# Kernel optimization log

Measured on AMD Instinct MI355X. Metric: run time of the kernel, lower is better.

The kernel has to match this reference:

```python
import jax, jax.numpy as jnp
import numpy as np

V = 100000   # vocab_size
D = 128      # d_model
N = 262144   # number of (target, context) training pairs
K = 5        # num_negatives


def setup_inputs() -> dict:
    key = jax.random.key(0)
    k1, k2, k3, k4, k5 = jax.random.split(key, 5)
    emb = jax.random.normal(k1, (V, D), dtype=jnp.float32)      # input embedding table
    out_w = jax.random.normal(k2, (V, D), dtype=jnp.float32)    # output (Linear) weight [V, D]
    tgt_ids = jax.random.randint(k3, (N,), 0, V)
    ctx_ids = jax.random.randint(k4, (N,), 0, V)
    neg_ids = jax.random.randint(k5, (N, K), 0, V)
    return {"emb": emb, "out_w": out_w, "tgt_ids": tgt_ids,
            "ctx_ids": ctx_ids, "neg_ids": neg_ids}


def reference(emb, out_w, tgt_ids, ctx_ids, neg_ids):
    # Batched skip-gram with negative sampling (SGNS), faithful to the
    # per-pair math in _train_skipgram:
    #   input_e = embeddings(tgt); pos_e = weight.weight[ctx]
    #   neg_e   = weight.weight[neg_ids]
    #   loss    = -(logsigmoid(<input_e, pos_e>) + sum logsigmoid(-neg_e @ input_e))
    input_e = emb[tgt_ids]            # [N, D]
    pos_e = out_w[ctx_ids]            # [N, D]
    neg_e = out_w[neg_ids]            # [N, K, D]

    pos_score = jnp.sum(input_e * pos_e, axis=-1)            # [N]
    neg_score = jnp.einsum('nkd,nd->nk', neg_e, input_e)     # [N, K]

    loss = -(jax.nn.log_sigmoid(pos_score)
             + jnp.sum(jax.nn.log_sigmoid(-neg_score), axis=-1))  # [N]
    return loss
```

## Files before the change

kernel.cpp:

```cpp
#include <hip/hip_runtime.h>
#include <hip/hip_fp16.h>
#include <math.h>


#define D 128
#define K 5

typedef _Float16 h2 __attribute__((ext_vector_type(2)));

__device__ __forceinline__ void sched_fence() {
#if __has_builtin(__builtin_amdgcn_sched_barrier)
    __builtin_amdgcn_sched_barrier(0);
#else
    asm volatile("" ::: "memory");
#endif
}

__device__ __forceinline__ float log_sigmoid(float x) {
    return fminf(x, 0.0f) - __logf(1.0f + __expf(-fabsf(x)));
}

__device__ __forceinline__ float dot8_f16(uint4 a, uint4 b, float acc) {
    acc = __builtin_amdgcn_fdot2(__builtin_bit_cast(h2, a.x),
                                 __builtin_bit_cast(h2, b.x), acc, false);
    acc = __builtin_amdgcn_fdot2(__builtin_bit_cast(h2, a.y),
                                 __builtin_bit_cast(h2, b.y), acc, false);
    acc = __builtin_amdgcn_fdot2(__builtin_bit_cast(h2, a.z),
                                 __builtin_bit_cast(h2, b.z), acc, false);
    acc = __builtin_amdgcn_fdot2(__builtin_bit_cast(h2, a.w),
                                 __builtin_bit_cast(h2, b.w), acc, false);
    return acc;
}

struct H8 { __half2 a, b, c, d; };

__global__ __launch_bounds__(256) void cvt2_f16_kernel(
    const float* __restrict__ src0, const float* __restrict__ src1,
    __half* __restrict__ dst0, __half* __restrict__ dst1, int n )
{
    int i = (blockIdx.x * blockDim.x + threadIdx.x) * 8;
    const float* src = src0;
    __half* dst = dst0;
    if (i >= n) { src = src1; dst = dst1; i -= n; }
    if (i >= n) return;
    float4 x = *(const float4*)(src + i);
    float4 y = *(const float4*)(src + i + 4);
    H8 h;
    h.a = __floats2half2_rn(x.x, x.y);
    h.b = __floats2half2_rn(x.z, x.w);
    h.c = __floats2half2_rn(y.x, y.y);
    h.d = __floats2half2_rn(y.z, y.w);
    *(H8*)(dst + i) = h;
}

__global__ __launch_bounds__(256) void sgns_f16_kernel(
    const __half* __restrict__ embh,
    const __half* __restrict__ outh,
    const int* __restrict__ tgt_ids,
    const int* __restrict__ ctx_ids,
    const int* __restrict__ neg_ids,
    float* __restrict__ out,
    int N)
{
    const int lane = threadIdx.x & 63;
    const int wave = threadIdx.x >> 6;
    const int lg   = lane & 15;
    const int grp  = lane >> 4;
    const int base = (blockIdx.x * 4 + wave) * 8;
    const int n0 = base + grp;
    const int n1 = n0 + 4;
    if (n0 >= N) return;

    const int t0 = tgt_ids[n0];
    const int t1 = tgt_ids[n1];
    int rowsA[K + 1], rowsB[K + 1];
    rowsA[0] = ctx_ids[n0];
    rowsB[0] = ctx_ids[n1];
    {
        const int4 a4 = *(const int4*)(neg_ids + (size_t)n0 * K);
        rowsA[1] = a4.x; rowsA[2] = a4.y; rowsA[3] = a4.z; rowsA[4] = a4.w;
        rowsA[5] = neg_ids[(size_t)n0 * K + 4];
        const int4 b4 = *(const int4*)(neg_ids + (size_t)n1 * K);
        rowsB[1] = b4.x; rowsB[2] = b4.y; rowsB[3] = b4.z; rowsB[4] = b4.w;
        rowsB[5] = neg_ids[(size_t)n1 * K + 4];
    }

    const uint4 inA = ((const uint4*)(embh + (size_t)t0 * D))[lg];
    const uint4 inB = ((const uint4*)(embh + (size_t)t1 * D))[lg];
    uint4 wA[K + 1], wB[K + 1];
#pragma unroll
    for (int j = 0; j < K + 1; ++j)
        wA[j] = ((const uint4*)(outh + (size_t)rowsA[j] * D))[lg];
#pragma unroll
    for (int j = 0; j < K + 1; ++j)
        wB[j] = ((const uint4*)(outh + (size_t)rowsB[j] * D))[lg];
    sched_fence();

    float dotA[K + 1], dotB[K + 1];
#pragma unroll
    for (int j = 0; j < K + 1; ++j)
        dotA[j] = dot8_f16(inA, wA[j], 0.0f);
#pragma unroll
    for (int j = 0; j < K + 1; ++j)
        dotB[j] = dot8_f16(inB, wB[j], 0.0f);

#pragma unroll
    for (int j = 0; j < K + 1; ++j) {
        float v = dotA[j];
        v += __shfl_xor(v, 1);
        v += __shfl_xor(v, 2);
        v += __shfl_xor(v, 4);
        v += __shfl_xor(v, 8);
        dotA[j] = v;
        float u = dotB[j];
        u += __shfl_xor(u, 1);
        u += __shfl_xor(u, 2);
        u += __shfl_xor(u, 4);
        u += __shfl_xor(u, 8);
        dotB[j] = u;
    }

    if (lg == 0) {
        float lossA = log_sigmoid(dotA[0]);
        float lossB = log_sigmoid(dotB[0]);
#pragma unroll
        for (int j = 1; j < K + 1; ++j) {
            lossA += log_sigmoid(-dotA[j]);
            lossB += log_sigmoid(-dotB[j]);
        }
        out[n0] = -lossA;
        out[n1] = -lossB;
    }
}

__global__ __launch_bounds__(256) void sgns_f32_kernel(
    const float* __restrict__ emb,
    const float* __restrict__ out_w,
    const int* __restrict__ tgt_ids,
    const int* __restrict__ ctx_ids,
    const int* __restrict__ neg_ids,
    float* __restrict__ out,
    int N)
{
    const int lane = threadIdx.x & 63;
    const int wave = threadIdx.x >> 6;
    const int lg   = lane & 15;
    const int grp  = lane >> 4;
    const int n = (blockIdx.x * 4 + wave) * 4 + grp;
    if (n >= N) return;

    const int t = tgt_ids[n];
    int rows[K + 1];
    rows[0] = ctx_ids[n];
    const int4 n4 = *(const int4*)(neg_ids + (size_t)n * K);
    rows[1] = n4.x; rows[2] = n4.y; rows[3] = n4.z; rows[4] = n4.w;
    rows[5] = neg_ids[(size_t)n * K + 4];

    const float4* er = (const float4*)(emb + (size_t)t * D);
    const float4 in0 = er[lg];
    const float4 in1 = er[lg + 16];

    float4 w0[K + 1], w1[K + 1];
#pragma unroll
    for (int j = 0; j < K + 1; ++j) {
        const float4* wr = (const float4*)(out_w + (size_t)rows[j] * D);
        w0[j] = wr[lg];
        w1[j] = wr[lg + 16];
    }

    float dot[K + 1];
#pragma unroll
    for (int j = 0; j < K + 1; ++j) {
        dot[j] = in0.x * w0[j].x + in0.y * w0[j].y
               + in0.z * w0[j].z + in0.w * w0[j].w
               + in1.x * w1[j].x + in1.y * w1[j].y
               + in1.z * w1[j].z + in1.w * w1[j].w;
    }

#pragma unroll
    for (int j = 0; j < K + 1; ++j) {
        float v = dot[j];
        v += __shfl_xor(v, 1);
        v += __shfl_xor(v, 2);
        v += __shfl_xor(v, 4);
        v += __shfl_xor(v, 8);
        dot[j] = v;
    }

    if (lg == 0) {
        float loss = log_sigmoid(dot[0]);
#pragma unroll
        for (int j = 1; j < K + 1; ++j)
            loss += log_sigmoid(-dot[j]);
        out[n] = -loss;
    }
}

extern "C" void kernel_launch(void* const* d_in, const int* in_sizes, int n_in,
                              void* d_out, int out_size, void* d_ws, size_t ws_size,
                              hipStream_t stream) {
    const float* emb     = (const float*)d_in[0];
    const float* out_w   = (const float*)d_in[1];
    const int*   tgt_ids = (const int*)d_in[2];
    const int*   ctx_ids = (const int*)d_in[3];
    const int*   neg_ids = (const int*)d_in[4];
    float* out = (float*)d_out;

    const int N = in_sizes[2];
    const size_t vd = (size_t)in_sizes[0];
    const size_t need = 2 * vd * sizeof(__half);

    if (ws_size >= need) {
        __half* embh = (__half*)d_ws;
        __half* outh = embh + vd;
        const int cvt_threads = (int)(2 * vd / 8);
        const int cvt_blocks = (cvt_threads + 255) / 256;
        cvt2_f16_kernel<<<cvt_blocks, 256, 0, stream>>>(emb, out_w, embh, outh,
                                                        (int)vd);
        const int blocks = (N + 31) / 32;
        sgns_f16_kernel<<<blocks, 256, 0, stream>>>(embh, outh, tgt_ids,
                                                    ctx_ids, neg_ids, out, N);
    } else {
        const int blocks = (N + 15) / 16;
        sgns_f32_kernel<<<blocks, 256, 0, stream>>>(emb, out_w, tgt_ids,
                                                    ctx_ids, neg_ids, out, N);
    }
}
```

Measured before the change: 191.5 us.

## Gather embedding rows via direct global-to-LDS loads, one pair per lane group

Replaces the register-based gather of f16 embedding rows with global_load_lds builtins that copy 16-byte fragments straight into per-wave shared memory, then reads them back from LDS for the fdot2 dot products. Each 16-lane group now handles one pair instead of two, so the grid doubles and out-of-range threads are clamped instead of returning early. The aim is to cut VGPR pressure and raise the number of loads in flight. The cost is 28 KB of LDS per block, which may cap occupancy, plus an extra LDS read pass and less per-thread memory-level parallelism.

```diff
diff --git a/kernel.cpp b/kernel.cpp
--- a/kernel.cpp
+++ b/kernel.cpp
@@ -7,14 +7,6 @@
 #define K 5
 
 typedef _Float16 h2 __attribute__((ext_vector_type(2)));
-
-__device__ __forceinline__ void sched_fence() {
-#if __has_builtin(__builtin_amdgcn_sched_barrier)
-    __builtin_amdgcn_sched_barrier(0);
-#else
-    asm volatile("" ::: "memory");
-#endif
-}
 
 __device__ __forceinline__ float log_sigmoid(float x) {
     return fminf(x, 0.0f) - __logf(1.0f + __expf(-fabsf(x)));
@@ -30,6 +22,13 @@
     acc = __builtin_amdgcn_fdot2(__builtin_bit_cast(h2, a.w),
                                  __builtin_bit_cast(h2, b.w), acc, false);
     return acc;
+}
+
+__device__ __forceinline__ void gload16(const void* gptr, void* lptr) {
+    __builtin_amdgcn_global_load_lds(
+        (const __attribute__((address_space(1))) void*)gptr,
+        (__attribute__((address_space(3))) void*)lptr,
+        16, 0, 0);
 }
 
 struct H8 { __half2 a, b, c, d; };
@@ -53,7 +52,7 @@
     *(H8*)(dst + i) = h;
 }
 
-__global__ __launch_bounds__(256) void sgns_f16_kernel(
+__global__ __launch_bounds__(256) void sgns_f16_lds_kernel(
     const __half* __restrict__ embh,
     const __half* __restrict__ outh,
     const int* __restrict__ tgt_ids,
@@ -62,74 +61,63 @@
     float* __restrict__ out,
     int N)
 {
+    __shared__ alignas(16) char smem[4 * 7 * 1024];
+
     const int lane = threadIdx.x & 63;
     const int wave = threadIdx.x >> 6;
     const int lg   = lane & 15;
     const int grp  = lane >> 4;
-    const int base = (blockIdx.x * 4 + wave) * 8;
-    const int n0 = base + grp;
-    const int n1 = n0 + 4;
-    if (n0 >= N) return;
-
-    const int t0 = tgt_ids[n0];
-    const int t1 = tgt_ids[n1];
-    int rowsA[K + 1], rowsB[K + 1];
-    rowsA[0] = ctx_ids[n0];
-    rowsB[0] = ctx_ids[n1];
+    const int n_raw = (blockIdx.x * 4 + wave) * 4 + grp;
+    const bool valid = n_raw < N;
+    const int n = valid ? n_raw : N - 1;
+
+    const int t = tgt_ids[n];
+    int rows[K + 1];
+    rows[0] = ctx_ids[n];
     {
-        const int4 a4 = *(const int4*)(neg_ids + (size_t)n0 * K);
-        rowsA[1] = a4.x; rowsA[2] = a4.y; rowsA[3] = a4.z; rowsA[4] = a4.w;
-        rowsA[5] = neg_ids[(size_t)n0 * K + 4];
-        const int4 b4 = *(const int4*)(neg_ids + (size_t)n1 * K);
-        rowsB[1] = b4.x; rowsB[2] = b4.y; rowsB[3] = b4.z; rowsB[4] = b4.w;
-        rowsB[5] = neg_ids[(size_t)n1 * K + 4];
-    }
-
-    const uint4 inA = ((const uint4*)(embh + (size_t)t0 * D))[lg];
-    const uint4 inB = ((const uint4*)(embh + (size_t)t1 * D))[lg];
-    uint4 wA[K + 1], wB[K + 1];
+        const int4 n4 = *(const int4*)(neg_ids + (size_t)n * K);
+        rows[1] = n4.x; rows[2] = n4.y; rows[3] = n4.z; rows[4] = n4.w;
+        rows[5] = neg_ids[(size_t)n * K + 4];
+    }
+
+    char* wbase = smem + wave * (7 * 1024);
+
+    gload16(embh + (size_t)t * D + lg * 8, wbase);
 #pragma unroll
     for (int j = 0; j < K + 1; ++j)
-        wA[j] = ((const uint4*)(outh + (size_t)rowsA[j] * D))[lg];
-#pragma unroll
-    for (int j = 0; j < K + 1; ++j)
-        wB[j] = ((const uint4*)(outh + (size_t)rowsB[j] * D))[lg];
-    sched_fence();
-
-    float dotA[K + 1], dotB[K + 1];
-#pragma unroll
-    for (int j = 0; j < K + 1; ++j)
-        dotA[j] = dot8_f16(inA, wA[j], 0.0f);
-#pragma unroll
-    for (int j = 0; j < K + 1; ++j)
-        dotB[j] = dot8_f16(inB, wB[j], 0.0f);
-
-#pragma unroll
-    for (int j = 0; j < K + 1; ++j) {
-        float v = dotA[j];
+        gload16(outh + (size_t)rows[j] * D + lg * 8,
+                wbase + (j + 1) * 1024);
+
+    asm volatile("s_waitcnt vmcnt(0)" ::: "memory");
+#if __has_builtin(__builtin_amdgcn_sched_barrier)
+    __builtin_amdgcn_sched_barrier(0);
+#endif
+
+    const char* myfrag = wbase + lane * 16;
+    const uint4 in = *(const uint4*)(myfrag);
+    float dot[K + 1];
+#pragma unroll
+    for (int j = 0; j < K + 1; ++j) {
+        const uint4 w = *(const uint4*)(myfrag + (j + 1) * 1024);
+        dot[j] = dot8_f16(in, w, 0.0f);
+    }
+
+#pragma unroll
+    for (int j = 0; j < K + 1; ++j) {
+        float v = dot[j];
         v += __shfl_xor(v, 1);
         v += __shfl_xor(v, 2);
         v += __shfl_xor(v, 4);
         v += __shfl_xor(v, 8);
-        dotA[j] = v;
-        float u = dotB[j];
-        u += __shfl_xor(u, 1);
-        u += __shfl_xor(u, 2);
-        u += __shfl_xor(u, 4);
-        u += __shfl_xor(u, 8);
-        dotB[j] = u;
-    }
-
-    if (lg == 0) {
-        float lossA = log_sigmoid(dotA[0]);
-        float lossB = log_sigmoid(dotB[0]);
-#pragma unroll
-        for (int j = 1; j < K + 1; ++j) {
-            lossA += log_sigmoid(-dotA[j]);
-            lossB += log_sigmoid(-dotB[j]);
-        }
-        out[n0] = -lossA;
-        out[n1] = -lossB;
+        dot[j] = v;
+    }
+
+    if (lg == 0 && valid) {
+        float loss = log_sigmoid(dot[0]);
+#pragma unroll
+        for (int j = 1; j < K + 1; ++j)
+            loss += log_sigmoid(-dot[j]);
+        out[n] = -loss;
     }
 }
 
@@ -217,9 +205,9 @@
         const int cvt_blocks = (cvt_threads + 255) / 256;
         cvt2_f16_kernel<<<cvt_blocks, 256, 0, stream>>>(emb, out_w, embh, outh,
                                                         (int)vd);
-        const int blocks = (N + 31) / 32;
-        sgns_f16_kernel<<<blocks, 256, 0, stream>>>(embh, outh, tgt_ids,
-                                                    ctx_ids, neg_ids, out, N);
+        const int blocks = (N + 15) / 16;
+        sgns_f16_lds_kernel<<<blocks, 256, 0, stream>>>(embh, outh, tgt_ids,
+                                                        ctx_ids, neg_ids, out, N);
     } else {
         const int blocks = (N + 15) / 16;
         sgns_f32_kernel<<<blocks, 256, 0, stream>>>(emb, out_w, tgt_ids,
```

Measured after the change: 190.5 us. No clear change (-0.5%).
